# Kernel tuning notes

Measured on AMD Instinct MI355X. Metric: run time of the kernel, lower is better.

Reference implementation:

```python
import jax, jax.numpy as jnp
import numpy as np

B, L, ENC, DEC, ATT = 256, 196, 2048, 512, 512

def setup_inputs() -> dict:
    key = jax.random.key(0)
    ks = jax.random.split(key, 8)
    s_enc = 1.0 / np.sqrt(ENC); s_dec = 1.0 / np.sqrt(DEC); s_att = 1.0 / np.sqrt(ATT)
    return {
        "encoder_out": jax.random.normal(ks[0], (B, L, ENC), dtype=jnp.float32),
        "decoder_hidden": jax.random.normal(ks[1], (B, DEC), dtype=jnp.float32),
        "W_enc": jax.random.uniform(ks[2], (ENC, ATT), jnp.float32, -s_enc, s_enc),
        "b_enc": jax.random.uniform(ks[3], (ATT,), jnp.float32, -s_enc, s_enc),
        "W_dec": jax.random.uniform(ks[4], (DEC, ATT), jnp.float32, -s_dec, s_dec),
        "b_dec": jax.random.uniform(ks[5], (ATT,), jnp.float32, -s_dec, s_dec),
        "W_att": jax.random.uniform(ks[6], (ATT, 1), jnp.float32, -s_att, s_att),
        "b_att": jax.random.uniform(ks[7], (1,), jnp.float32, -s_att, s_att),
    }

def reference(encoder_out, decoder_hidden, W_enc, b_enc, W_dec, b_dec, W_att, b_att):
    # encoder_att: [B, L, A]; decoder_att: [B, A]
    encoder_att = jnp.einsum('ble,ea->bla', encoder_out, W_enc) + b_enc
    decoder_att = decoder_hidden @ W_dec + b_dec
    hidden = jax.nn.relu(encoder_att + decoder_att[:, None, :])  # [B, L, A]
    att = jnp.einsum('bla,a->bl', hidden, W_att[:, 0]) + b_att[0]  # [B, L]
    alpha = jax.nn.softmax(att, axis=1)  # softmax over sequence dim
    awe = jnp.einsum('ble,bl->be', encoder_out, alpha)  # weighted sum
    return awe, alpha
```

## Files before the change

### kernel.cpp

```cpp
#include <hip/hip_runtime.h>
#include <hip/hip_bf16.h>
#include <stdint.h>

#define NB 256
#define NL 196
#define NE 2048
#define ND 512
#define NA 512
#define NM (NB * NL)

typedef __attribute__((ext_vector_type(4))) float f32x4;
typedef __attribute__((ext_vector_type(8))) short bf16x8;

static __device__ __forceinline__ unsigned short f2bf(float f) {
  __hip_bfloat16 h = __float2bfloat16(f);
  unsigned short u;
  __builtin_memcpy(&u, &h, 2);
  return u;
}

__global__ __launch_bounds__(512) void k_prep(
    const float* __restrict__ W, unsigned short* __restrict__ Bp,
    const float* __restrict__ dec, const float* __restrict__ Wd,
    const float* __restrict__ bd, const float* __restrict__ be,
    float* __restrict__ d2) {
  if (blockIdx.x < 256) {
    int t = blockIdx.x * 512 + threadIdx.x;
    int lane = t & 63;
    int kt32 = (t >> 6) & 63;
    int ntile = t >> 12;
    int col = ntile * 16 + (lane & 15);
    int k0 = kt32 * 32 + ((lane >> 4) << 3);
    bf16x8 o;
#pragma unroll
    for (int j = 0; j < 8; ++j) o[j] = (short)f2bf(W[(size_t)(k0 + j) * NA + col]);
    *reinterpret_cast<bf16x8*>(Bp + ((size_t)t << 3)) = o;
  } else {
    __shared__ float dh[8][ND];
    const int b0 = (blockIdx.x - 256) * 8, tid = threadIdx.x;
#pragma unroll
    for (int j = 0; j < 8; ++j) dh[j][tid] = dec[(size_t)(b0 + j) * ND + tid];
    __syncthreads();
    float base = bd[tid] + be[tid];
    float acc[8];
#pragma unroll
    for (int j = 0; j < 8; ++j) acc[j] = base;
#pragma unroll 4
    for (int e = 0; e < ND; ++e) {
      float w = Wd[(size_t)e * NA + tid];
#pragma unroll
      for (int j = 0; j < 8; ++j) acc[j] = fmaf(dh[j][e], w, acc[j]);
    }
#pragma unroll
    for (int j = 0; j < 8; ++j) d2[(size_t)(b0 + j) * NA + tid] = acc[j];
  }
}

#define BM 64
#define BK 64
#define KT (NE / BK)

__global__ __launch_bounds__(512, 4) void k_main(
    const float* __restrict__ A,
    const unsigned short* __restrict__ Bp,
    const float* __restrict__ d2,
    const float* __restrict__ Watt,
    const float* __restrict__ batt,
    float* __restrict__ att)
{
  __shared__ unsigned short As[2][BM * BK];
  __shared__ float att_w[8][BM];

  const int tid = threadIdx.x;
  const int lane = tid & 63;
  const int wid = tid >> 6;
  const int lq = lane >> 4;
  const int lr = lane & 15;
  const int row0 = blockIdx.x * BM;

  f32x4 acc[4][4];
#pragma unroll
  for (int mf = 0; mf < 4; ++mf)
#pragma unroll
    for (int r = 0; r < 4; ++r) {
      int rowg = row0 + mf * 16 + lq * 4 + r;
      int bb = rowg / NL;
      const float* d2r = d2 + (size_t)bb * NA + wid * 64 + lr;
#pragma unroll
      for (int nf = 0; nf < 4; ++nf) acc[mf][nf][r] = d2r[nf * 16];
    }

  const int srow = tid >> 3;
  const int skc = tid & 7;
  const float* ag = A + (size_t)(row0 + srow) * NE + skc * 8;
  const int swz_w = srow * 64 + ((skc ^ (srow & 7)) << 3);

  f32x4 s0, s1;
  auto cvt_store = [&](int buf) {
    bf16x8 o;
    o[0] = (short)f2bf(s0[0]); o[1] = (short)f2bf(s0[1]);
    o[2] = (short)f2bf(s0[2]); o[3] = (short)f2bf(s0[3]);
    o[4] = (short)f2bf(s1[0]); o[5] = (short)f2bf(s1[1]);
    o[6] = (short)f2bf(s1[2]); o[7] = (short)f2bf(s1[3]);
    *reinterpret_cast<bf16x8*>(&As[buf][swz_w]) = o;
  };

  s0 = *reinterpret_cast<const f32x4*>(ag);
  s1 = *reinterpret_cast<const f32x4*>(ag + 4);
  cvt_store(0);
  __syncthreads();

  const unsigned short* bpw = Bp + (size_t)(wid * 4) * 32768 + lane * 8;

  for (int kt = 0; kt < KT; ++kt) {
    const int cur = kt & 1;
    bf16x8 bf[2][4];
#pragma unroll
    for (int ks = 0; ks < 2; ++ks)
#pragma unroll
      for (int nf = 0; nf < 4; ++nf)
        bf[ks][nf] = *reinterpret_cast<const bf16x8*>(bpw + (size_t)nf * 32768 + (size_t)(kt * 2 + ks) * 512);
    if (kt + 1 < KT) {
      const float* agn = ag + (size_t)(kt + 1) * BK;
      s0 = *reinterpret_cast<const f32x4*>(agn);
      s1 = *reinterpret_cast<const f32x4*>(agn + 4);
    }
#pragma unroll
    for (int ks = 0; ks < 2; ++ks)
#pragma unroll
      for (int mf = 0; mf < 4; ++mf) {
        const int rrow = mf * 16 + lr;
        const int chunk = (ks * 4 + lq) ^ (lr & 7);
        bf16x8 af = *reinterpret_cast<const bf16x8*>(&As[cur][rrow * 64 + (chunk << 3)]);
#pragma unroll
        for (int nf = 0; nf < 4; ++nf)
          acc[mf][nf] = __builtin_amdgcn_mfma_f32_16x16x32_bf16(af, bf[ks][nf], acc[mf][nf], 0, 0, 0);
      }
    if (kt + 1 < KT) cvt_store(cur ^ 1);
    __syncthreads();
  }

  float w[4];
#pragma unroll
  for (int nf = 0; nf < 4; ++nf) w[nf] = Watt[wid * 64 + nf * 16 + lr];
#pragma unroll
  for (int mf = 0; mf < 4; ++mf)
#pragma unroll
    for (int r = 0; r < 4; ++r) {
      float s = 0.f;
#pragma unroll
      for (int nf = 0; nf < 4; ++nf) s = fmaf(fmaxf(acc[mf][nf][r], 0.f), w[nf], s);
      s += __shfl_xor(s, 1);
      s += __shfl_xor(s, 2);
      s += __shfl_xor(s, 4);
      s += __shfl_xor(s, 8);
      if (lr == 0) att_w[wid][mf * 16 + lq * 4 + r] = s;
    }
  __syncthreads();
  if (tid < BM) {
    float s = 0.f;
#pragma unroll
    for (int wv = 0; wv < 8; ++wv) s += att_w[wv][tid];
    att[row0 + tid] = s + batt[0];
  }
}

__global__ __launch_bounds__(256) void k_awe(
    const float* __restrict__ enc, const float* __restrict__ att,
    float* __restrict__ alpha_out, float* __restrict__ awe) {
  __shared__ float al[256];
  const int b = blockIdx.x >> 1, ch = blockIdx.x & 1, tid = threadIdx.x;

  if (tid < 64) {
    const int lane = tid;
    const float* ar = att + (size_t)b * NL;
    float v[4];
#pragma unroll
    for (int i = 0; i < 4; ++i) {
      int l = i * 64 + lane;
      v[i] = (l < NL) ? ar[l] : -1e30f;
    }
    float m = fmaxf(fmaxf(v[0], v[1]), fmaxf(v[2], v[3]));
#pragma unroll
    for (int o = 32; o >= 1; o >>= 1) m = fmaxf(m, __shfl_xor(m, o));
    float e[4];
    float s = 0.f;
#pragma unroll
    for (int i = 0; i < 4; ++i) {
      int l = i * 64 + lane;
      e[i] = (l < NL) ? __expf(v[i] - m) : 0.f;
      s += e[i];
    }
#pragma unroll
    for (int o = 32; o >= 1; o >>= 1) s += __shfl_xor(s, o);
    float inv = 1.f / s;
#pragma unroll
    for (int i = 0; i < 4; ++i) {
      int l = i * 64 + lane;
      if (l < NL) {
        float a = e[i] * inv;
        al[l] = a;
        if (ch == 0) alpha_out[(size_t)b * NL + l] = a;
      }
    }
  }
  __syncthreads();

  const float* ep = enc + (size_t)b * NL * NE + ch * 1024 + tid * 4;
  f32x4 a0 = {0.f, 0.f, 0.f, 0.f}, a1 = a0, a2 = a0, a3 = a0;
#pragma unroll 2
  for (int l = 0; l < NL; l += 4) {
    f32x4 v0 = *reinterpret_cast<const f32x4*>(ep + (size_t)l * NE);
    f32x4 v1 = *reinterpret_cast<const f32x4*>(ep + (size_t)(l + 1) * NE);
    f32x4 v2 = *reinterpret_cast<const f32x4*>(ep + (size_t)(l + 2) * NE);
    f32x4 v3 = *reinterpret_cast<const f32x4*>(ep + (size_t)(l + 3) * NE);
    float c0 = al[l], c1 = al[l + 1], c2 = al[l + 2], c3 = al[l + 3];
#pragma unroll
    for (int j = 0; j < 4; ++j) {
      a0[j] = fmaf(c0, v0[j], a0[j]);
      a1[j] = fmaf(c1, v1[j], a1[j]);
      a2[j] = fmaf(c2, v2[j], a2[j]);
      a3[j] = fmaf(c3, v3[j], a3[j]);
    }
  }
  f32x4 s4;
#pragma unroll
  for (int j = 0; j < 4; ++j) s4[j] = (a0[j] + a1[j]) + (a2[j] + a3[j]);
  *reinterpret_cast<f32x4*>(awe + (size_t)b * NE + ch * 1024 + tid * 4) = s4;
}

extern "C" void kernel_launch(void* const* d_in, const int* in_sizes, int n_in,
                              void* d_out, int out_size, void* d_ws, size_t ws_size,
                              hipStream_t stream) {
  const float* enc  = (const float*)d_in[0];
  const float* dec  = (const float*)d_in[1];
  const float* Wenc = (const float*)d_in[2];
  const float* benc = (const float*)d_in[3];
  const float* Wdec = (const float*)d_in[4];
  const float* bdec = (const float*)d_in[5];
  const float* Watt = (const float*)d_in[6];
  const float* batt = (const float*)d_in[7];

  float* awe   = (float*)d_out;
  float* alpha = (float*)d_out + (size_t)NB * NE;

  char* ws = (char*)d_ws;
  unsigned short* Bp = (unsigned short*)ws;
  float* d2  = (float*)(ws + (size_t)2 * 1024 * 1024);
  float* att = (float*)(ws + (size_t)2 * 1024 * 1024 + 512 * 1024);

  k_prep<<<dim3(288), dim3(512), 0, stream>>>(Wenc, Bp, dec, Wdec, bdec, benc, d2);
  k_main<<<dim3(NM / BM), dim3(512), 0, stream>>>(enc, Bp, d2, Watt, batt, att);
  k_awe<<<dim3(NB * 2), dim3(256), 0, stream>>>(enc, att, alpha, awe);
}
```

Baseline: 286.4 us.

## Double M-tile to 128 rows with 16 waves and replicate packed weights per XCD

The main GEMM block doubles from 64 to 128 rows using 1024 threads arranged as 2x8 waves, so each staged bf16 weight fragment is shared by twice as many A rows. The prep kernel writes 8 copies of the packed W_enc and each block reads the copy chosen by blockIdx&7, likely to spread weight traffic across per-XCD L2 caches. B-fragment loads move inside the ks loop to reduce register pressure. Risks: fewer blocks (392), a 1024-thread block limiting occupancy, and extra prep writes and workspace for the replicas.

```diff
diff --git a/kernel.cpp b/kernel.cpp
--- a/kernel.cpp
+++ b/kernel.cpp
@@ -8,6 +8,8 @@
 #define ND 512
 #define NA 512
 #define NM (NB * NL)
+
+#define BPCOPY (1u << 20)
 
 typedef __attribute__((ext_vector_type(4))) float f32x4;
 typedef __attribute__((ext_vector_type(8))) short bf16x8;
@@ -34,7 +36,9 @@
     bf16x8 o;
 #pragma unroll
     for (int j = 0; j < 8; ++j) o[j] = (short)f2bf(W[(size_t)(k0 + j) * NA + col]);
-    *reinterpret_cast<bf16x8*>(Bp + ((size_t)t << 3)) = o;
+#pragma unroll
+    for (int x = 0; x < 8; ++x)
+      *reinterpret_cast<bf16x8*>(Bp + (size_t)x * BPCOPY + ((size_t)t << 3)) = o;
   } else {
     __shared__ float dh[8][ND];
     const int b0 = (blockIdx.x - 256) * 8, tid = threadIdx.x;
@@ -56,11 +60,11 @@
   }
 }
 
-#define BM 64
+#define BM 128
 #define BK 64
 #define KT (NE / BK)
 
-__global__ __launch_bounds__(512, 4) void k_main(
+__global__ __launch_bounds__(1024, 4) void k_main(
     const float* __restrict__ A,
     const unsigned short* __restrict__ Bp,
     const float* __restrict__ d2,
@@ -74,6 +78,8 @@
   const int tid = threadIdx.x;
   const int lane = tid & 63;
   const int wid = tid >> 6;
+  const int wr = wid >> 3;
+  const int wc = wid & 7;
   const int lq = lane >> 4;
   const int lr = lane & 15;
   const int row0 = blockIdx.x * BM;
@@ -83,9 +89,9 @@
   for (int mf = 0; mf < 4; ++mf)
 #pragma unroll
     for (int r = 0; r < 4; ++r) {
-      int rowg = row0 + mf * 16 + lq * 4 + r;
+      int rowg = row0 + wr * 64 + mf * 16 + lq * 4 + r;
       int bb = rowg / NL;
-      const float* d2r = d2 + (size_t)bb * NA + wid * 64 + lr;
+      const float* d2r = d2 + (size_t)bb * NA + wc * 64 + lr;
 #pragma unroll
       for (int nf = 0; nf < 4; ++nf) acc[mf][nf][r] = d2r[nf * 16];
     }
@@ -93,7 +99,7 @@
   const int srow = tid >> 3;
   const int skc = tid & 7;
   const float* ag = A + (size_t)(row0 + srow) * NE + skc * 8;
-  const int swz_w = srow * 64 + ((skc ^ (srow & 7)) << 3);
+  const int swz_w = srow * BK + ((skc ^ (srow & 7)) << 3);
 
   f32x4 s0, s1;
   auto cvt_store = [&](int buf) {
@@ -110,39 +116,39 @@
   cvt_store(0);
   __syncthreads();
 
-  const unsigned short* bpw = Bp + (size_t)(wid * 4) * 32768 + lane * 8;
+  const unsigned short* bpw = Bp + (size_t)(blockIdx.x & 7) * BPCOPY
+                                 + (size_t)(wc * 4) * 32768 + lane * 8;
 
   for (int kt = 0; kt < KT; ++kt) {
     const int cur = kt & 1;
-    bf16x8 bf[2][4];
-#pragma unroll
-    for (int ks = 0; ks < 2; ++ks)
-#pragma unroll
-      for (int nf = 0; nf < 4; ++nf)
-        bf[ks][nf] = *reinterpret_cast<const bf16x8*>(bpw + (size_t)nf * 32768 + (size_t)(kt * 2 + ks) * 512);
     if (kt + 1 < KT) {
       const float* agn = ag + (size_t)(kt + 1) * BK;
       s0 = *reinterpret_cast<const f32x4*>(agn);
       s1 = *reinterpret_cast<const f32x4*>(agn + 4);
     }
 #pragma unroll
-    for (int ks = 0; ks < 2; ++ks)
+    for (int ks = 0; ks < 2; ++ks) {
+      bf16x8 bf[4];
+#pragma unroll
+      for (int nf = 0; nf < 4; ++nf)
+        bf[nf] = *reinterpret_cast<const bf16x8*>(bpw + (size_t)nf * 32768 + (size_t)(kt * 2 + ks) * 512);
 #pragma unroll
       for (int mf = 0; mf < 4; ++mf) {
-        const int rrow = mf * 16 + lr;
+        const int rrow = wr * 64 + mf * 16 + lr;
         const int chunk = (ks * 4 + lq) ^ (lr & 7);
-        bf16x8 af = *reinterpret_cast<const bf16x8*>(&As[cur][rrow * 64 + (chunk << 3)]);
+        bf16x8 af = *reinterpret_cast<const bf16x8*>(&As[cur][rrow * BK + (chunk << 3)]);
 #pragma unroll
         for (int nf = 0; nf < 4; ++nf)
-          acc[mf][nf] = __builtin_amdgcn_mfma_f32_16x16x32_bf16(af, bf[ks][nf], acc[mf][nf], 0, 0, 0);
+          acc[mf][nf] = __builtin_amdgcn_mfma_f32_16x16x32_bf16(af, bf[nf], acc[mf][nf], 0, 0, 0);
       }
+    }
     if (kt + 1 < KT) cvt_store(cur ^ 1);
     __syncthreads();
   }
 
   float w[4];
 #pragma unroll
-  for (int nf = 0; nf < 4; ++nf) w[nf] = Watt[wid * 64 + nf * 16 + lr];
+  for (int nf = 0; nf < 4; ++nf) w[nf] = Watt[wc * 64 + nf * 16 + lr];
 #pragma unroll
   for (int mf = 0; mf < 4; ++mf)
 #pragma unroll
@@ -154,7 +160,7 @@
       s += __shfl_xor(s, 2);
       s += __shfl_xor(s, 4);
       s += __shfl_xor(s, 8);
-      if (lr == 0) att_w[wid][mf * 16 + lq * 4 + r] = s;
+      if (lr == 0) att_w[wc][wr * 64 + mf * 16 + lq * 4 + r] = s;
     }
   __syncthreads();
   if (tid < BM) {
@@ -246,10 +252,10 @@
 
   char* ws = (char*)d_ws;
   unsigned short* Bp = (unsigned short*)ws;
-  float* d2  = (float*)(ws + (size_t)2 * 1024 * 1024);
-  float* att = (float*)(ws + (size_t)2 * 1024 * 1024 + 512 * 1024);
+  float* d2  = (float*)(ws + (size_t)16 * 1024 * 1024);
+  float* att = (float*)(ws + (size_t)16 * 1024 * 1024 + 512 * 1024);
 
   k_prep<<<dim3(288), dim3(512), 0, stream>>>(Wenc, Bp, dec, Wdec, bdec, benc, d2);
-  k_main<<<dim3(NM / BM), dim3(512), 0, stream>>>(enc, Bp, d2, Watt, batt, att);
+  k_main<<<dim3(NM / BM), dim3(1024), 0, stream>>>(enc, Bp, d2, Watt, batt, att);
   k_awe<<<dim3(NB * 2), dim3(256), 0, stream>>>(enc, att, alpha, awe);
 }
```

Result: slower. 316.5 us (+10.5%).
